# Kernel optimization log

Hardware: AMD Instinct MI355X
Metric: run time of the kernel (lower is better)

## Reference

```python
import jax, jax.numpy as jnp
import numpy as np

B, N, D = 4, 2048, 1024
WIN, K, ALPHA = 4, 8, 0.3


def setup_inputs() -> dict:
    key = jax.random.key(0)
    ks = jax.random.split(key, 16)
    s_d = 1.0 / np.sqrt(D)
    s_2d = 1.0 / np.sqrt(2 * D)
    inp = {
        'mu': jax.random.normal(ks[0], (B, N, D), jnp.float32),
        'pheromone': jax.random.uniform(ks[1], (B, N), jnp.float32),
        'Wq': jax.random.normal(ks[2], (D, D), jnp.float32) * s_d,
        'bq': jnp.zeros((D,), jnp.float32),
        'Wk': jax.random.normal(ks[3], (D, D), jnp.float32) * s_d,
        'bk': jnp.zeros((D,), jnp.float32),
        'Wv': jax.random.normal(ks[4], (D, D), jnp.float32) * s_d,
        'bv': jnp.zeros((D,), jnp.float32),
        'Wm1': jax.random.normal(ks[5], (2 * D, D), jnp.float32) * s_2d,
        'bm1': jnp.zeros((D,), jnp.float32),
        'Wm2': jax.random.normal(ks[6], (D, D), jnp.float32) * s_d,
        'bm2': jnp.zeros((D,), jnp.float32),
        'Wo': jax.random.normal(ks[7], (2 * D, D), jnp.float32) * s_2d,
        'bo': jnp.zeros((D,), jnp.float32),
    }
    return inp


def reference(mu, pheromone, Wq, bq, Wk, bk, Wv, bv, Wm1, bm1, Wm2, bm2, Wo, bo):
    # ---- local windowed gather-MLP ----
    padded = jnp.pad(mu, ((0, 0), (WIN, 0), (0, 0)))  # causal left-pad
    neighbors = jnp.stack([padded[:, WIN - w:WIN - w + N, :] for w in range(1, WIN + 1)], axis=2)
    self_exp = jnp.broadcast_to(mu[:, :, None, :], neighbors.shape)
    cat = jnp.concatenate([self_exp, neighbors], axis=-1)
    h = jax.nn.silu(cat @ Wm1 + bm1) @ Wm2 + bm2
    local_msgs = h.mean(axis=2)  # (B,N,D)

    # ---- causal top-k attention with pheromone bias ----
    q = mu @ Wq + bq
    k = mu @ Wk + bk
    v = mu @ Wv + bv
    scale = 1.0 / jnp.sqrt(jnp.asarray(D, mu.dtype))
    scores = jnp.einsum('bnd,bmd->bnm', q, k) * scale  # (B,N,N)
    scores = scores + ALPHA * pheromone[:, None, :]
    row = jnp.arange(N)
    causal = jnp.where(row[None, :] > row[:, None], -jnp.inf, 0.0).astype(mu.dtype)
    scores = scores + causal[None]
    # top-k sparsification (N > K): softmax over the k kept scores, zeros elsewhere
    vals, idx = jax.lax.top_k(scores, K)  # (B,N,K)
    probs = jax.nn.softmax(vals, axis=-1)
    bi = jnp.arange(B)[:, None, None]
    ni = jnp.arange(N)[None, :, None]
    attn = jnp.zeros_like(scores).at[bi, ni, idx].set(probs)
    global_msgs = jnp.einsum('bnm,bmd->bnd', attn, v)

    return jnp.concatenate([local_msgs, global_msgs], axis=-1) @ Wo + bo
```

## Files before the change

### kernel.cpp

```cpp
#include <hip/hip_runtime.h>
#include <hip/hip_bf16.h>
#include <math.h>

#define B_ 4
#define N_ 2048
#define D_ 1024
#define WIN_ 4
#define KTOP 8
#define ALPHA_ 0.3f
#define SCALE_ (1.0f/32.0f)
#define NCH 16
#define INV2048 0.00048828125f

typedef unsigned short ushortT;
typedef _Float16 halfT;
typedef __attribute__((ext_vector_type(8))) _Float16 half8v;
typedef __attribute__((ext_vector_type(4))) float f32x4;

__device__ inline ushortT h2u(halfT h){ union{halfT h; ushortT u;} x; x.h=h; return x.u; }
__device__ inline halfT  u2h(ushortT u){ union{halfT h; ushortT u;} x; x.u=u; return x.h; }
__device__ inline float  uh2f(ushortT u){ return (float)u2h(u); }

__device__ __forceinline__ void gll16(const ushortT* g, ushortT* l) {
    __builtin_amdgcn_global_load_lds(
        (const __attribute__((address_space(1))) void*)g,
        (__attribute__((address_space(3))) void*)l, 16, 0, 0);
}

__global__ __launch_bounds__(256)
void prep_all(const float* __restrict__ mu, const float* __restrict__ Wm1,
              const float* __restrict__ Wm2, const float* __restrict__ Wv,
              const float* __restrict__ Wo, const float* __restrict__ Wq,
              const float* __restrict__ Wk,
              ushortT* __restrict__ mu_a, ushortT* __restrict__ mu_B,
              ushortT* __restrict__ WtF, ushortT* __restrict__ Wt_m2,
              ushortT* __restrict__ Wt_v, ushortT* __restrict__ Wt_o,
              ushortT* __restrict__ WqT_a, ushortT* __restrict__ WqT_B,
              ushortT* __restrict__ WkT_a, ushortT* __restrict__ WkT_B)
{
    const int bid = blockIdx.x;
    if (bid < 8192) {
        size_t base = ((size_t)bid * 256 + threadIdx.x) * 4;
        float4 v = *reinterpret_cast<const float4*>(&mu[base]);
        float vv[4] = {v.x, v.y, v.z, v.w};
        ushort4 pa, pb;
#pragma unroll
        for (int j = 0; j < 4; ++j) {
            float f = vv[j];
            halfT a = (halfT)f;  float r = f - (float)a;
            halfT b = (halfT)(r * 2048.0f);
            ((ushortT*)&pa)[j] = h2u(a); ((ushortT*)&pb)[j] = h2u(b);
        }
        *reinterpret_cast<ushort4*>(&mu_a[base]) = pa;
        *reinterpret_cast<ushort4*>(&mu_B[base]) = pb;
        return;
    }
    __shared__ float t[32][33];
    int b = bid - 8192;
    const float* W; ushortT* Pa; ushortT* Pb = nullptr;
    int K, lb, split = 0;
    if (b < 1024)      { W = Wm1;                       Pa = WtF;                     K = 1024; lb = b; }
    else if (b < 2048) { W = Wm1 + (size_t)1024 * 1024; Pa = WtF + (size_t)1024*1024; K = 1024; lb = b - 1024; }
    else if (b < 3072) { W = Wm2;  Pa = Wt_m2; K = 1024; lb = b - 2048; }
    else if (b < 4096) { W = Wv;   Pa = Wt_v;  K = 1024; lb = b - 3072; }
    else if (b < 6144) { W = Wo;   Pa = Wt_o;  K = 2048; lb = b - 4096; }
    else if (b < 7168) { W = Wq;   Pa = WqT_a; Pb = WqT_B; K = 1024; lb = b - 6144; split = 1; }
    else               { W = Wk;   Pa = WkT_a; Pb = WkT_B; K = 1024; lb = b - 7168; split = 1; }
    const int Nn = 1024;
    const int k0 = (K == 2048) ? (lb & 63) * 32 : (lb & 31) * 32;
    const int n0 = (K == 2048) ? (lb >> 6) * 32 : (lb >> 5) * 32;
    const int tx = threadIdx.x & 31, ty8 = threadIdx.x >> 5;
#pragma unroll
    for (int p = 0; p < 4; ++p) {
        int kk = p * 8 + ty8;
        t[kk][tx] = W[(size_t)(k0 + kk) * Nn + n0 + tx];
    }
    __syncthreads();
#pragma unroll
    for (int p = 0; p < 4; ++p) {
        int nn = p * 8 + ty8;
        float f = t[tx][nn];
        size_t o = (size_t)(n0 + nn) * K + k0 + tx;
        if (split) {
            halfT a = (halfT)f;  float r = f - (float)a;
            halfT bb = (halfT)(r * 2048.0f);
            Pa[o] = h2u(a); Pb[o] = h2u(bb);
        } else {
            Pa[o] = h2u((halfT)f);
        }
    }
}

__device__ __forceinline__ void gemm_core_h(
    const ushortT* __restrict__ A, int lda, const ushortT* __restrict__ Bt, int ldb,
    const float* __restrict__ bias, void* __restrict__ Cout, int ldc, int K,
    int m0, int n0, int outHalf, ushortT* AsL, ushortT* BsL)
{
    const int tid = threadIdx.x;
    const int w = tid >> 6, lane = tid & 63;
    const int wr = w >> 1, wc = w & 1;

    f32x4 acc[4][4];
#pragma unroll
    for (int mi = 0; mi < 4; ++mi)
#pragma unroll
        for (int ni = 0; ni < 4; ++ni) acc[mi][ni] = (f32x4){0.f, 0.f, 0.f, 0.f};

    for (int k0 = 0; k0 < K; k0 += 64) {
#pragma unroll
        for (int it = 0; it < 4; ++it) {
            int idx = tid + it * 256;
            int row = idx >> 3, c = idx & 7;
            int4 va = *reinterpret_cast<const int4*>(&A[(size_t)(m0 + row) * lda + k0 + c * 8]);
            *reinterpret_cast<int4*>(&AsL[row * 72 + c * 8]) = va;
            int4 vb = *reinterpret_cast<const int4*>(&Bt[(size_t)(n0 + row) * ldb + k0 + c * 8]);
            *reinterpret_cast<int4*>(&BsL[row * 72 + c * 8]) = vb;
        }
        __syncthreads();
#pragma unroll
        for (int kh = 0; kh < 2; ++kh) {
            const int ko = kh * 32 + (lane >> 4) * 8;
            const int rr = lane & 15;
            half8v af[4], bf[4];
#pragma unroll
            for (int mi = 0; mi < 4; ++mi)
                af[mi] = *reinterpret_cast<const half8v*>(&AsL[(wr * 64 + mi * 16 + rr) * 72 + ko]);
#pragma unroll
            for (int ni = 0; ni < 4; ++ni)
                bf[ni] = *reinterpret_cast<const half8v*>(&BsL[(wc * 64 + ni * 16 + rr) * 72 + ko]);
#pragma unroll
            for (int mi = 0; mi < 4; ++mi)
#pragma unroll
                for (int ni = 0; ni < 4; ++ni)
                    acc[mi][ni] = __builtin_amdgcn_mfma_f32_16x16x32_f16(
                        af[mi], bf[ni], acc[mi][ni], 0, 0, 0);
        }
        __syncthreads();
    }

    const int r4 = (lane >> 4) * 4, cl = lane & 15;
#pragma unroll
    for (int mi = 0; mi < 4; ++mi)
#pragma unroll
        for (int ni = 0; ni < 4; ++ni) {
            int row = m0 + wr * 64 + mi * 16 + r4;
            int col = n0 + wc * 64 + ni * 16 + cl;
            float bb = bias ? bias[col] : 0.f;
#pragma unroll
            for (int r = 0; r < 4; ++r) {
                float v = acc[mi][ni][r] + bb;
                if (outHalf)
                    ((ushortT*)Cout)[(size_t)(row + r) * ldc + col] = h2u((halfT)v);
                else
                    ((float*)Cout)[(size_t)(row + r) * ldc + col] = v;
            }
        }
}

template<int OUT_HALF>
__global__ __launch_bounds__(256)
void mfma_gemm_h(const ushortT* __restrict__ A, int lda,
                 const ushortT* __restrict__ Bt, int ldb,
                 const float* __restrict__ bias,
                 void* __restrict__ Cout, int ldc, int K)
{
    __shared__ ushortT AsL[128 * 72];
    __shared__ ushortT BsL[128 * 72];
    gemm_core_h(A, lda, Bt, ldb, bias, Cout, ldc, K,
                blockIdx.y * 128, blockIdx.x * 128, OUT_HALF, AsL, BsL);
}

__global__ __launch_bounds__(256)
void gemm_pf_v(const ushortT* __restrict__ mu_a,
               const ushortT* __restrict__ WtF, const ushortT* __restrict__ Wt_v,
               const float* __restrict__ bv,
               float* __restrict__ PF, ushortT* __restrict__ Vb16)
{
    __shared__ ushortT AsL[128 * 72];
    __shared__ ushortT BsL[128 * 72];
    const int bid = blockIdx.x;
    if (bid < 1024) {
        gemm_core_h(mu_a, D_, WtF, D_, (const float*)nullptr, (void*)PF, 2 * D_, D_,
                    (bid >> 4) * 128, (bid & 15) * 128, 0, AsL, BsL);
    } else {
        const int b2 = bid - 1024;
        gemm_core_h(mu_a, D_, Wt_v, D_, bv, (void*)Vb16, D_, D_,
                    (b2 >> 3) * 128, (b2 & 7) * 128, 1, AsL, BsL);
    }
}

__global__ __launch_bounds__(256)
void silu_mean(const float* __restrict__ P, const float* __restrict__ bm1,
               ushortT* __restrict__ Sb)
{
    size_t idx4 = (size_t)blockIdx.x * blockDim.x + threadIdx.x;
    size_t base = idx4 << 2;
    int row = (int)(base >> 10);
    int col = (int)(base & 1023);
    int n = row & (N_ - 1);
    float4 a = *reinterpret_cast<const float4*>(&P[(size_t)row * 2048 + col]);
    float4 bb = *reinterpret_cast<const float4*>(&bm1[col]);
    a.x += bb.x; a.y += bb.y; a.z += bb.z; a.w += bb.w;
    float sx = 0.f, sy = 0.f, sz = 0.f, sw = 0.f;
#pragma unroll
    for (int w = 1; w <= WIN_; ++w) {
        float xx = a.x, xy = a.y, xz = a.z, xw = a.w;
        if (n >= w) {
            const float4 nb = *reinterpret_cast<const float4*>(
                &P[(size_t)(row - w) * 2048 + 1024 + col]);
            xx += nb.x; xy += nb.y; xz += nb.z; xw += nb.w;
        }
        sx += xx / (1.f + __expf(-xx));
        sy += xy / (1.f + __expf(-xy));
        sz += xz / (1.f + __expf(-xz));
        sw += xw / (1.f + __expf(-xw));
    }
    ushort4 o = {h2u((halfT)(sx * 0.25f)), h2u((halfT)(sy * 0.25f)),
                 h2u((halfT)(sz * 0.25f)), h2u((halfT)(sw * 0.25f))};
    *reinterpret_cast<ushort4*>(&Sb[base]) = o;
}

__device__ inline void topk_insert(float (&tv)[KTOP], int (&ti)[KTOP], float s, int m)
{
    if ((s > tv[KTOP-1]) || (s == tv[KTOP-1] && m < ti[KTOP-1])) {
        float cs = s; int ci = m;
#pragma unroll
        for (int q = 0; q < KTOP; ++q) {
            bool beats = (cs > tv[q]) || (cs == tv[q] && ci < ti[q]);
            if (beats) { float t0 = tv[q]; int t1 = ti[q];
                         tv[q] = cs; ti[q] = ci; cs = t0; ci = t1; }
        }
    }
}

#define SPLIT3H_COMPUTE(Tb, wr, wc, lane, acc0, acc1)                           \
    {                                                                           \
        const int rr_ = (lane) & 15, q_ = (lane) >> 4;                          \
        const int Rb0_ = (wc) * 32 + rr_;                                       \
        const int Rb1_ = Rb0_ + 16;                                             \
        half8v ba0_ = *reinterpret_cast<const half8v*>(                         \
            &Tb[2 * 4096 + Rb0_ * 32 + ((q_ ^ ((Rb0_ >> 1) & 3)) << 3)]);       \
        half8v ba1_ = *reinterpret_cast<const half8v*>(                         \
            &Tb[2 * 4096 + Rb1_ * 32 + ((q_ ^ ((Rb1_ >> 1) & 3)) << 3)]);       \
        half8v bB0_ = *reinterpret_cast<const half8v*>(                         \
            &Tb[3 * 4096 + Rb0_ * 32 + ((q_ ^ ((Rb0_ >> 1) & 3)) << 3)]);       \
        half8v bB1_ = *reinterpret_cast<const half8v*>(                         \
            &Tb[3 * 4096 + Rb1_ * 32 + ((q_ ^ ((Rb1_ >> 1) & 3)) << 3)]);       \
        _Pragma("unroll")                                                       \
        for (int mi_ = 0; mi_ < 4; ++mi_) {                                     \
            const int Ra_ = (wr) * 64 + mi_ * 16 + rr_;                         \
            const int sw_ = (q_ ^ ((Ra_ >> 1) & 3)) << 3;                       \
            half8v aA_ = *reinterpret_cast<const half8v*>(&Tb[Ra_ * 32 + sw_]); \
            acc0[mi_][0] = __builtin_amdgcn_mfma_f32_16x16x32_f16(              \
                aA_, ba0_, acc0[mi_][0], 0, 0, 0);                              \
            acc0[mi_][1] = __builtin_amdgcn_mfma_f32_16x16x32_f16(              \
                aA_, ba1_, acc0[mi_][1], 0, 0, 0);                              \
            acc1[mi_][0] = __builtin_amdgcn_mfma_f32_16x16x32_f16(              \
                aA_, bB0_, acc1[mi_][0], 0, 0, 0);                              \
            acc1[mi_][1] = __builtin_amdgcn_mfma_f32_16x16x32_f16(              \
                aA_, bB1_, acc1[mi_][1], 0, 0, 0);                              \
        }                                                                       \
        _Pragma("unroll")                                                       \
        for (int mi_ = 0; mi_ < 4; ++mi_) {                                     \
            const int Ra_ = (wr) * 64 + mi_ * 16 + rr_;                         \
            const int sw_ = (q_ ^ ((Ra_ >> 1) & 3)) << 3;                       \
            half8v aB_ = *reinterpret_cast<const half8v*>(                      \
                &Tb[4096 + Ra_ * 32 + sw_]);                                    \
            acc1[mi_][0] = __builtin_amdgcn_mfma_f32_16x16x32_f16(              \
                aB_, ba0_, acc1[mi_][0], 0, 0, 0);                              \
            acc1[mi_][1] = __builtin_amdgcn_mfma_f32_16x16x32_f16(              \
                aB_, ba1_, acc1[mi_][1], 0, 0, 0);                              \
        }                                                                       \
    }

#define STAGE4(lb, koff)                                                        \
    {                                                                           \
        gll16(gp + goff + (koff), lb);                                          \
        gll16(gp + goff + (koff) + 16 * D_, (lb) + 512);                        \
        gll16(gp + goff + (koff) + 32 * D_, (lb) + 1024);                       \
        gll16(gp + goff + (koff) + 48 * D_, (lb) + 1536);                       \
    }

__global__ __launch_bounds__(512, 2)
void mid_all(const ushortT* __restrict__ A0, const ushortT* __restrict__ A1,
             const ushortT* __restrict__ QWa, const ushortT* __restrict__ QWB,
             const ushortT* __restrict__ KWa, const ushortT* __restrict__ KWB,
             const float* __restrict__ bq, const float* __restrict__ bk,
             ushortT* __restrict__ Qa, ushortT* __restrict__ QB,
             ushortT* __restrict__ Ka, ushortT* __restrict__ KB,
             const ushortT* __restrict__ Sb, const ushortT* __restrict__ Wt_m2,
             const float* __restrict__ bm2, ushortT* __restrict__ CCb)
{
    __shared__ ushortT SMEM[18432];

    const int tid = threadIdx.x;
    const int wid = tid >> 6, lane = tid & 63;

    if (blockIdx.x >= 1024) {
        const int t = blockIdx.x - 1024;
        const int m0 = (t >> 3) * 128;
        const int n0 = (t & 7) * 128;
        ushortT* AsL = SMEM;
        ushortT* BsL = SMEM + 9216;
        const int wr = wid >> 2, wc = wid & 3;

        f32x4 acc[4][2];
#pragma unroll
        for (int mi = 0; mi < 4; ++mi) { acc[mi][0] = (f32x4){0,0,0,0}; acc[mi][1] = (f32x4){0,0,0,0}; }

        for (int k0 = 0; k0 < D_; k0 += 64) {
#pragma unroll
            for (int it = 0; it < 2; ++it) {
                int idx = tid + it * 512;
                int row = idx >> 3, c = idx & 7;
                int4 va = *reinterpret_cast<const int4*>(&Sb[(size_t)(m0 + row) * D_ + k0 + c * 8]);
                *reinterpret_cast<int4*>(&AsL[row * 72 + c * 8]) = va;
                int4 vb = *reinterpret_cast<const int4*>(&Wt_m2[(size_t)(n0 + row) * D_ + k0 + c * 8]);
                *reinterpret_cast<int4*>(&BsL[row * 72 + c * 8]) = vb;
            }
            __syncthreads();
#pragma unroll
            for (int kh = 0; kh < 2; ++kh) {
                const int ko = kh * 32 + (lane >> 4) * 8;
                const int rr = lane & 15;
                half8v af[4], bf[2];
#pragma unroll
                for (int mi = 0; mi < 4; ++mi)
                    af[mi] = *reinterpret_cast<const half8v*>(&AsL[(wr * 64 + mi * 16 + rr) * 72 + ko]);
#pragma unroll
                for (int ni = 0; ni < 2; ++ni)
                    bf[ni] = *reinterpret_cast<const half8v*>(&BsL[(wc * 32 + ni * 16 + rr) * 72 + ko]);
#pragma unroll
                for (int mi = 0; mi < 4; ++mi)
#pragma unroll
                    for (int ni = 0; ni < 2; ++ni)
                        acc[mi][ni] = __builtin_amdgcn_mfma_f32_16x16x32_f16(
                            af[mi], bf[ni], acc[mi][ni], 0, 0, 0);
            }
            __syncthreads();
        }

        const int r4 = (lane >> 4) * 4, cl = lane & 15;
#pragma unroll
        for (int mi = 0; mi < 4; ++mi)
#pragma unroll
            for (int ni = 0; ni < 2; ++ni) {
                int col = n0 + wc * 32 + ni * 16 + cl;
                float bb = bm2[col];
#pragma unroll
                for (int r = 0; r < 4; ++r) {
                    int row = m0 + wr * 64 + mi * 16 + r4 + r;
                    CCb[(size_t)row * 2048 + col] = h2u((halfT)(acc[mi][ni][r] + bb));
                }
            }
        return;
    }

    ushortT* TT = SMEM;
    const int half = blockIdx.x >> 9;
    int lin = blockIdx.x & 511;
    lin = (lin & 7) * 64 + (lin >> 3);
    const int m0 = (lin >> 3) * 128;
    const int n0 = (lin & 7) * 128;

    const ushortT* B0 = half ? KWa : QWa;
    const ushortT* B1 = half ? KWB : QWB;
    const float* bias = half ? bk : bq;
    ushortT* Pa = half ? Ka : Qa;
    ushortT* Pb = half ? KB : QB;

    const int wr = wid >> 2, wc = wid & 3;
    const int pl = wid >> 1;
    const int hb = (wid & 1) * 64;
    const ushortT* gp = (pl == 0) ? A0 : (pl == 1) ? A1 : (pl == 2) ? B0 : B1;
    const int rbase = (pl < 2 ? m0 : n0) + hb + (lane >> 2);
    const int cg8 = ((lane & 3) ^ ((lane >> 3) & 3)) << 3;
    const size_t goff = (size_t)rbase * D_ + cg8;
    ushortT* lb0 = &TT[pl * 4096 + hb * 32];

    f32x4 acc0[4][2], acc1[4][2];
#pragma unroll
    for (int mi = 0; mi < 4; ++mi) {
        acc0[mi][0] = (f32x4){0,0,0,0}; acc0[mi][1] = (f32x4){0,0,0,0};
        acc1[mi][0] = (f32x4){0,0,0,0}; acc1[mi][1] = (f32x4){0,0,0,0};
    }

    for (int ks = 0; ks < 32; ++ks) {
        STAGE4(lb0, (size_t)ks * 32)
        __syncthreads();
        __builtin_amdgcn_s_setprio(1);
        SPLIT3H_COMPUTE(TT, wr, wc, lane, acc0, acc1)
        __builtin_amdgcn_s_setprio(0);
        __syncthreads();
    }

    const int r4 = (lane >> 4) * 4, cl = lane & 15;
#pragma unroll
    for (int mi = 0; mi < 4; ++mi)
#pragma unroll
        for (int ni = 0; ni < 2; ++ni) {
            int col = n0 + wc * 32 + ni * 16 + cl;
            float bb = bias[col];
#pragma unroll
            for (int r = 0; r < 4; ++r) {
                int row = m0 + wr * 64 + mi * 16 + r4 + r;
                float v = acc0[mi][ni][r] + INV2048 * acc1[mi][ni][r] + bb;
                halfT a = (halfT)v;  float r1 = v - (float)a;
                halfT b = (halfT)(r1 * 2048.0f);
                size_t o = (size_t)row * D_ + col;
                Pa[o] = h2u(a); Pb[o] = h2u(b);
            }
        }
}

__global__ __launch_bounds__(512, 2)
void attn_scores_h(const ushortT* __restrict__ Qa, const ushortT* __restrict__ QB,
                   const ushortT* __restrict__ Ka, const ushortT* __restrict__ KB,
                   const float* __restrict__ pher,
                   float* __restrict__ WV, int* __restrict__ WI)
{
    __shared__ ushortT TT[16384];
    __shared__ float Ps[128];
    __shared__ float PV[32 * 4 * 8];
    __shared__ int   PI[32 * 4 * 8];
    float* MV = reinterpret_cast<float*>(&TT[0]);
    int*   MI = reinterpret_cast<int*>((char*)&TT[0] + 16384);

    int lin = blockIdx.y * 136 + blockIdx.x;
    lin = (lin & 7) * 68 + (lin >> 3);
    const int b = lin / 136;
    const int xy = lin - b * 136;
    int g = 0;
    while ((g + 1) * (g + 2) / 2 <= xy) ++g;
    const int ch = xy - g * (g + 1) / 2;
    const int n0 = g * 128;
    const int m0 = ch * 128;
    const size_t bN = (size_t)b * N_;

    const int tid = threadIdx.x;
    const int wid = tid >> 6, lane = tid & 63;
    const int wr = wid >> 2, wc = wid & 3;

    if (tid < 128) Ps[tid] = pher[bN + m0 + tid];

    const int pl = wid >> 1;
    const int hb = (wid & 1) * 64;
    const ushortT* gp = (pl == 0) ? Qa : (pl == 1) ? QB : (pl == 2) ? Ka : KB;
    const size_t rbase = bN + (pl < 2 ? n0 : m0) + hb + (lane >> 2);
    const int cg8 = ((lane & 3) ^ ((lane >> 3) & 3)) << 3;
    const size_t goff = rbase * (size_t)D_ + cg8;
    ushortT* lb0 = &TT[pl * 4096 + hb * 32];

    f32x4 acc0[4][2], acc1[4][2];
#pragma unroll
    for (int mi = 0; mi < 4; ++mi) {
        acc0[mi][0] = (f32x4){0,0,0,0}; acc0[mi][1] = (f32x4){0,0,0,0};
        acc1[mi][0] = (f32x4){0,0,0,0}; acc1[mi][1] = (f32x4){0,0,0,0};
    }

    for (int ks = 0; ks < 32; ++ks) {
        STAGE4(lb0, (size_t)ks * 32)
        __syncthreads();
        __builtin_amdgcn_s_setprio(1);
        SPLIT3H_COMPUTE(TT, wr, wc, lane, acc0, acc1)
        __builtin_amdgcn_s_setprio(0);
        __syncthreads();
    }

    const int r4 = (lane >> 4) * 4, cl = lane & 15;
    for (int p = 0; p < 4; ++p) {
        __syncthreads();
        if (wr == (p >> 1)) {
#pragma unroll
            for (int mi2 = 0; mi2 < 2; ++mi2) {
                const int mi = (p & 1) * 2 + mi2;
#pragma unroll
                for (int ni = 0; ni < 2; ++ni) {
                    int col = wc * 32 + ni * 16 + cl;
                    int m = m0 + col;
#pragma unroll
                    for (int r = 0; r < 4; ++r) {
                        int rloc = mi2 * 16 + r4 + r;
                        int n = n0 + p * 32 + rloc;
                        bool ok = (m <= n);
                        float sc = acc0[mi][ni][r] + INV2048 * acc1[mi][ni][r];
                        MV[rloc * 128 + col] = ok ? (sc * SCALE_ + ALPHA_ * Ps[col])
                                                  : -INFINITY;
                        MI[rloc * 128 + col] = ok ? m : 0x7fffffff;
                    }
                }
            }
        }
        __syncthreads();
        if (tid < 128) {
            const int row = tid >> 2, q4 = tid & 3;
            float tv[KTOP]; int ti[KTOP];
#pragma unroll
            for (int j = 0; j < KTOP; ++j) { tv[j] = -INFINITY; ti[j] = 0x7fffffff; }
            for (int j = 0; j < 32; ++j) {
                float s2 = MV[row * 128 + q4 * 32 + j];
                if (s2 == -INFINITY) continue;
                topk_insert(tv, ti, s2, MI[row * 128 + q4 * 32 + j]);
            }
#pragma unroll
            for (int j = 0; j < KTOP; ++j) {
                PV[(row * 4 + q4) * 8 + j] = tv[j];
                PI[(row * 4 + q4) * 8 + j] = ti[j];
            }
        }
        __syncthreads();
        if (tid < 32) {
            float tv[KTOP]; int ti[KTOP];
#pragma unroll
            for (int j = 0; j < KTOP; ++j) { tv[j] = -INFINITY; ti[j] = 0x7fffffff; }
            for (int i = 0; i < 32; ++i) {
                float s2 = PV[tid * 32 + i];
                if (s2 == -INFINITY) continue;
                topk_insert(tv, ti, s2, PI[tid * 32 + i]);
            }
            int n = n0 + p * 32 + tid;
            size_t base = ((bN + n) * NCH + ch) * 8;
#pragma unroll
            for (int j = 0; j < KTOP; ++j) { WV[base + j] = tv[j]; WI[base + j] = ti[j]; }
        }
    }
}

__global__ __launch_bounds__(256)
void attn_merge(const float* __restrict__ WV, const int* __restrict__ WI,
                const ushortT* __restrict__ V, ushortT* __restrict__ CCb)
{
    __shared__ float CV[4][128];
    __shared__ int   CI[4][128];
    __shared__ float Pp[4][KTOP];
    __shared__ int   Pi[4][KTOP];

    const int tid  = threadIdx.x;
    const int wv   = tid >> 6;
    const int lane = tid & 63;
    const int rid  = blockIdx.x * 4 + wv;
    const int b    = rid >> 11;
    const int n    = rid & (N_ - 1);
    const int ncand = ((n >> 7) + 1) * 8;
    const size_t cbase = (size_t)rid * (NCH * 8);

#pragma unroll
    for (int t = 0; t < 2; ++t) {
        int i = lane + t * 64;
        if (i < ncand) { CV[wv][i] = WV[cbase + i]; CI[wv][i] = WI[cbase + i]; }
        else           { CV[wv][i] = -INFINITY;     CI[wv][i] = 0x7fffffff;   }
    }
    __syncthreads();

    if (lane == 0) {
        float tv[KTOP]; int ti[KTOP];
#pragma unroll
        for (int j = 0; j < KTOP; ++j) { tv[j] = -INFINITY; ti[j] = 0x7fffffff; }
        for (int i = 0; i < 128; ++i) {
            float s = CV[wv][i];
            if (s == -INFINITY) continue;
            topk_insert(tv, ti, s, CI[wv][i]);
        }
        float mx = tv[0];
        float e[KTOP]; float sum = 0.f;
#pragma unroll
        for (int j = 0; j < KTOP; ++j) {
            e[j] = (tv[j] == -INFINITY) ? 0.f : __expf(tv[j] - mx);
            sum += e[j];
        }
        float inv = 1.f / sum;
#pragma unroll
        for (int j = 0; j < KTOP; ++j) {
            Pp[wv][j] = e[j] * inv;
            Pi[wv][j] = (tv[j] == -INFINITY) ? 0 : ti[j];
        }
    }
    __syncthreads();

    const size_t vbase = (size_t)b * N_ * D_;
#pragma unroll
    for (int it = 0; it < 2; ++it) {
        int c8 = (it * 64 + lane) * 8;
        float o[8];
#pragma unroll
        for (int u = 0; u < 8; ++u) o[u] = 0.f;
#pragma unroll
        for (int j = 0; j < KTOP; ++j) {
            float p = Pp[wv][j];
            ushort4 v0 = *reinterpret_cast<const ushort4*>(
                &V[vbase + (size_t)Pi[wv][j] * D_ + c8]);
            ushort4 v1 = *reinterpret_cast<const ushort4*>(
                &V[vbase + (size_t)Pi[wv][j] * D_ + c8 + 4]);
            o[0] = fmaf(p, uh2f(v0.x), o[0]); o[1] = fmaf(p, uh2f(v0.y), o[1]);
            o[2] = fmaf(p, uh2f(v0.z), o[2]); o[3] = fmaf(p, uh2f(v0.w), o[3]);
            o[4] = fmaf(p, uh2f(v1.x), o[4]); o[5] = fmaf(p, uh2f(v1.y), o[5]);
            o[6] = fmaf(p, uh2f(v1.z), o[6]); o[7] = fmaf(p, uh2f(v1.w), o[7]);
        }
        ushort4 ob0 = {h2u((halfT)o[0]), h2u((halfT)o[1]), h2u((halfT)o[2]), h2u((halfT)o[3])};
        ushort4 ob1 = {h2u((halfT)o[4]), h2u((halfT)o[5]), h2u((halfT)o[6]), h2u((halfT)o[7])};
        *reinterpret_cast<ushort4*>(&CCb[(size_t)rid * 2048 + 1024 + c8]) = ob0;
        *reinterpret_cast<ushort4*>(&CCb[(size_t)rid * 2048 + 1024 + c8 + 4]) = ob1;
    }
}

extern "C" void kernel_launch(void* const* d_in, const int* in_sizes, int n_in,
                              void* d_out, int out_size, void* d_ws, size_t ws_size,
                              hipStream_t stream)
{
    const float* mu   = (const float*)d_in[0];
    const float* pher = (const float*)d_in[1];
    const float* Wq   = (const float*)d_in[2];
    const float* bq   = (const float*)d_in[3];
    const float* Wk   = (const float*)d_in[4];
    const float* bk   = (const float*)d_in[5];
    const float* Wv   = (const float*)d_in[6];
    const float* bv   = (const float*)d_in[7];
    const float* Wm1  = (const float*)d_in[8];
    const float* bm1  = (const float*)d_in[9];
    const float* Wm2  = (const float*)d_in[10];
    const float* bm2  = (const float*)d_in[11];
    const float* Wo   = (const float*)d_in[12];
    const float* bo   = (const float*)d_in[13];
    float* out = (float*)d_out;
    float* ws  = (float*)d_ws;

    const size_t SZ  = (size_t)B_ * N_ * D_;
    const size_t MEG = 1024 * 1024;
    const int M = B_ * N_;

    ushortT* CCb  = (ushortT*)ws;
    float*   PF   = ws + SZ;
    ushortT* Qa   = (ushortT*)(ws + SZ);
    ushortT* QB   = Qa + SZ;
    ushortT* Ka   = (ushortT*)(ws + 2 * SZ);
    ushortT* KB   = Ka + SZ;
    ushortT* mu_a = (ushortT*)(ws + 3 * SZ);
    ushortT* mu_B = mu_a + SZ;
    ushortT* Sb   = (ushortT*)(ws + 4 * SZ);
    float*   WVb  = (float*)(ws + 4 * SZ);
    int*     WIb  = (int*)(WVb + MEG);
    ushortT* Vb16 = (ushortT*)(ws + 4 * SZ + 4 * MEG);
    ushortT* U    = (ushortT*)(ws + 4 * SZ + 8 * MEG);
    ushortT* WtF  = U;
    ushortT* Wt_m2 = U + 2 * MEG;
    ushortT* Wt_v  = U + 3 * MEG;
    ushortT* WqT_a = U + 4 * MEG;        ushortT* WqT_B = U + 5 * MEG;
    ushortT* WkT_a = U + 6 * MEG;        ushortT* WkT_B = U + 7 * MEG;
    ushortT* Wt_o  = U + 8 * MEG;

    dim3 blk256(256), blk512(512);
    dim3 gD(8, 64);

    hipLaunchKernelGGL(prep_all, dim3(16384), blk256, 0, stream,
                       mu, Wm1, Wm2, Wv, Wo, Wq, Wk,
                       mu_a, mu_B, WtF, Wt_m2, Wt_v, Wt_o,
                       WqT_a, WqT_B, WkT_a, WkT_B);
    hipLaunchKernelGGL(gemm_pf_v, dim3(1536), blk256, 0, stream,
                       mu_a, WtF, Wt_v, bv, PF, Vb16);
    hipLaunchKernelGGL(silu_mean, dim3(SZ / 4 / 256), blk256, 0, stream, PF, bm1, Sb);
    hipLaunchKernelGGL(mid_all, dim3(1536), blk512, 0, stream,
                       mu_a, mu_B, WqT_a, WqT_B, WkT_a, WkT_B,
                       bq, bk, Qa, QB, Ka, KB,
                       Sb, Wt_m2, bm2, CCb);
    hipLaunchKernelGGL(attn_scores_h, dim3(136, B_), blk512, 0, stream,
                       Qa, QB, Ka, KB, pher, WVb, WIb);
    hipLaunchKernelGGL(attn_merge, dim3(M / 4), blk256, 0, stream, WVb, WIb, Vb16, CCb);
    hipLaunchKernelGGL((mfma_gemm_h<0>), gD, blk256, 0, stream,
                       CCb, 2 * D_, Wt_o, 2048, bo, (void*)out, D_, 2 * D_);

    (void)in_sizes; (void)n_in; (void)out_size; (void)ws_size;
}
```

Before: 739.1 us.

## Load MFMA operands directly from global memory instead of staging through LDS

```diff
diff --git a/kernel.cpp b/kernel.cpp
--- a/kernel.cpp
+++ b/kernel.cpp
@@ -20,12 +20,6 @@
 __device__ inline ushortT h2u(halfT h){ union{halfT h; ushortT u;} x; x.h=h; return x.u; }
 __device__ inline halfT  u2h(ushortT u){ union{halfT h; ushortT u;} x; x.u=u; return x.h; }
 __device__ inline float  uh2f(ushortT u){ return (float)u2h(u); }
-
-__device__ __forceinline__ void gll16(const ushortT* g, ushortT* l) {
-    __builtin_amdgcn_global_load_lds(
-        (const __attribute__((address_space(1))) void*)g,
-        (__attribute__((address_space(3))) void*)l, 16, 0, 0);
-}
 
 __global__ __launch_bounds__(256)
 void prep_all(const float* __restrict__ mu, const float* __restrict__ Wm1,
@@ -233,52 +227,37 @@
     }
 }
 
-#define SPLIT3H_COMPUTE(Tb, wr, wc, lane, acc0, acc1)                           \
+#define SPLIT3H_DIRECT(PA0, PA1, PB0, PB1, oA, oBv0, oBv1, kk, acc0, acc1)      \
     {                                                                           \
-        const int rr_ = (lane) & 15, q_ = (lane) >> 4;                          \
-        const int Rb0_ = (wc) * 32 + rr_;                                       \
-        const int Rb1_ = Rb0_ + 16;                                             \
-        half8v ba0_ = *reinterpret_cast<const half8v*>(                         \
-            &Tb[2 * 4096 + Rb0_ * 32 + ((q_ ^ ((Rb0_ >> 1) & 3)) << 3)]);       \
-        half8v ba1_ = *reinterpret_cast<const half8v*>(                         \
-            &Tb[2 * 4096 + Rb1_ * 32 + ((q_ ^ ((Rb1_ >> 1) & 3)) << 3)]);       \
-        half8v bB0_ = *reinterpret_cast<const half8v*>(                         \
-            &Tb[3 * 4096 + Rb0_ * 32 + ((q_ ^ ((Rb0_ >> 1) & 3)) << 3)]);       \
-        half8v bB1_ = *reinterpret_cast<const half8v*>(                         \
-            &Tb[3 * 4096 + Rb1_ * 32 + ((q_ ^ ((Rb1_ >> 1) & 3)) << 3)]);       \
+        half8v ba0_ = *reinterpret_cast<const half8v*>(&PB0[oBv0 + (kk)]);      \
+        half8v ba1_ = *reinterpret_cast<const half8v*>(&PB0[oBv1 + (kk)]);      \
+        half8v bB0_ = *reinterpret_cast<const half8v*>(&PB1[oBv0 + (kk)]);      \
+        half8v bB1_ = *reinterpret_cast<const half8v*>(&PB1[oBv1 + (kk)]);      \
+        half8v aA_[4], aB_[4];                                                  \
+        _Pragma("unroll")                                                       \
+        for (int mi_ = 0; mi_ < 4; ++mi_)                                       \
+            aA_[mi_] = *reinterpret_cast<const half8v*>(&PA0[oA[mi_] + (kk)]);  \
+        _Pragma("unroll")                                                       \
+        for (int mi_ = 0; mi_ < 4; ++mi_)                                       \
+            aB_[mi_] = *reinterpret_cast<const half8v*>(&PA1[oA[mi_] + (kk)]);  \
         _Pragma("unroll")                                                       \
         for (int mi_ = 0; mi_ < 4; ++mi_) {                                     \
-            const int Ra_ = (wr) * 64 + mi_ * 16 + rr_;                         \
-            const int sw_ = (q_ ^ ((Ra_ >> 1) & 3)) << 3;                       \
-            half8v aA_ = *reinterpret_cast<const half8v*>(&Tb[Ra_ * 32 + sw_]); \
             acc0[mi_][0] = __builtin_amdgcn_mfma_f32_16x16x32_f16(              \
-                aA_, ba0_, acc0[mi_][0], 0, 0, 0);                              \
+                aA_[mi_], ba0_, acc0[mi_][0], 0, 0, 0);                         \
             acc0[mi_][1] = __builtin_amdgcn_mfma_f32_16x16x32_f16(              \
-                aA_, ba1_, acc0[mi_][1], 0, 0, 0);                              \
+                aA_[mi_], ba1_, acc0[mi_][1], 0, 0, 0);                         \
             acc1[mi_][0] = __builtin_amdgcn_mfma_f32_16x16x32_f16(              \
-                aA_, bB0_, acc1[mi_][0], 0, 0, 0);                              \
+                aA_[mi_], bB0_, acc1[mi_][0], 0, 0, 0);                         \
             acc1[mi_][1] = __builtin_amdgcn_mfma_f32_16x16x32_f16(              \
-                aA_, bB1_, acc1[mi_][1], 0, 0, 0);                              \
+                aA_[mi_], bB1_, acc1[mi_][1], 0, 0, 0);                         \
         }                                                                       \
         _Pragma("unroll")                                                       \
         for (int mi_ = 0; mi_ < 4; ++mi_) {                                     \
-            const int Ra_ = (wr) * 64 + mi_ * 16 + rr_;                         \
-            const int sw_ = (q_ ^ ((Ra_ >> 1) & 3)) << 3;                       \
-            half8v aB_ = *reinterpret_cast<const half8v*>(                      \
-                &Tb[4096 + Ra_ * 32 + sw_]);                                    \
             acc1[mi_][0] = __builtin_amdgcn_mfma_f32_16x16x32_f16(              \
-                aB_, ba0_, acc1[mi_][0], 0, 0, 0);                              \
+                aB_[mi_], ba0_, acc1[mi_][0], 0, 0, 0);                         \
             acc1[mi_][1] = __builtin_amdgcn_mfma_f32_16x16x32_f16(              \
-                aB_, ba1_, acc1[mi_][1], 0, 0, 0);                              \
+                aB_[mi_], ba1_, acc1[mi_][1], 0, 0, 0);                         \
         }                                                                       \
-    }
-
-#define STAGE4(lb, koff)                                                        \
-    {                                                                           \
-        gll16(gp + goff + (koff), lb);                                          \
-        gll16(gp + goff + (koff) + 16 * D_, (lb) + 512);                        \
-        gll16(gp + goff + (koff) + 32 * D_, (lb) + 1024);                       \
-        gll16(gp + goff + (koff) + 48 * D_, (lb) + 1536);                       \
     }
 
 __global__ __launch_bounds__(512, 2)
@@ -356,7 +335,6 @@
         return;
     }
 
-    ushortT* TT = SMEM;
     const int half = blockIdx.x >> 9;
     int lin = blockIdx.x & 511;
     lin = (lin & 7) * 64 + (lin >> 3);
@@ -370,13 +348,13 @@
     ushortT* Pb = half ? KB : QB;
 
     const int wr = wid >> 2, wc = wid & 3;
-    const int pl = wid >> 1;
-    const int hb = (wid & 1) * 64;
-    const ushortT* gp = (pl == 0) ? A0 : (pl == 1) ? A1 : (pl == 2) ? B0 : B1;
-    const int rbase = (pl < 2 ? m0 : n0) + hb + (lane >> 2);
-    const int cg8 = ((lane & 3) ^ ((lane >> 3) & 3)) << 3;
-    const size_t goff = (size_t)rbase * D_ + cg8;
-    ushortT* lb0 = &TT[pl * 4096 + hb * 32];
+    const int rr = lane & 15, q8 = (lane >> 4) * 8;
+    size_t oA[4];
+#pragma unroll
+    for (int mi = 0; mi < 4; ++mi)
+        oA[mi] = (size_t)(m0 + wr * 64 + mi * 16 + rr) * D_ + q8;
+    const size_t oBv0 = (size_t)(n0 + wc * 32 + rr) * D_ + q8;
+    const size_t oBv1 = oBv0 + (size_t)16 * D_;
 
     f32x4 acc0[4][2], acc1[4][2];
 #pragma unroll
@@ -386,12 +364,8 @@
     }
 
     for (int ks = 0; ks < 32; ++ks) {
-        STAGE4(lb0, (size_t)ks * 32)
-        __syncthreads();
-        __builtin_amdgcn_s_setprio(1);
-        SPLIT3H_COMPUTE(TT, wr, wc, lane, acc0, acc1)
-        __builtin_amdgcn_s_setprio(0);
-        __syncthreads();
+        const int kk = ks * 32;
+        SPLIT3H_DIRECT(A0, A1, B0, B1, oA, oBv0, oBv1, kk, acc0, acc1)
     }
 
     const int r4 = (lane >> 4) * 4, cl = lane & 15;
@@ -419,12 +393,11 @@
                    const float* __restrict__ pher,
                    float* __restrict__ WV, int* __restrict__ WI)
 {
-    __shared__ ushortT TT[16384];
+    __shared__ float MV[32 * 128];
+    __shared__ int   MI[32 * 128];
     __shared__ float Ps[128];
     __shared__ float PV[32 * 4 * 8];
     __shared__ int   PI[32 * 4 * 8];
-    float* MV = reinterpret_cast<float*>(&TT[0]);
-    int*   MI = reinterpret_cast<int*>((char*)&TT[0] + 16384);
 
     int lin = blockIdx.y * 136 + blockIdx.x;
     lin = (lin & 7) * 68 + (lin >> 3);
@@ -443,13 +416,13 @@
 
     if (tid < 128) Ps[tid] = pher[bN + m0 + tid];
 
-    const int pl = wid >> 1;
-    const int hb = (wid & 1) * 64;
-    const ushortT* gp = (pl == 0) ? Qa : (pl == 1) ? QB : (pl == 2) ? Ka : KB;
-    const size_t rbase = bN + (pl < 2 ? n0 : m0) + hb + (lane >> 2);
-    const int cg8 = ((lane & 3) ^ ((lane >> 3) & 3)) << 3;
-    const size_t goff = rbase * (size_t)D_ + cg8;
-    ushortT* lb0 = &TT[pl * 4096 + hb * 32];
+    const int rr = lane & 15, q8 = (lane >> 4) * 8;
+    size_t oA[4];
+#pragma unroll
+    for (int mi = 0; mi < 4; ++mi)
+        oA[mi] = (bN + n0 + wr * 64 + mi * 16 + rr) * (size_t)D_ + q8;
+    const size_t oBv0 = (bN + m0 + wc * 32 + rr) * (size_t)D_ + q8;
+    const size_t oBv1 = oBv0 + (size_t)16 * D_;
 
     f32x4 acc0[4][2], acc1[4][2];
 #pragma unroll
@@ -459,12 +432,8 @@
     }
 
     for (int ks = 0; ks < 32; ++ks) {
-        STAGE4(lb0, (size_t)ks * 32)
-        __syncthreads();
-        __builtin_amdgcn_s_setprio(1);
-        SPLIT3H_COMPUTE(TT, wr, wc, lane, acc0, acc1)
-        __builtin_amdgcn_s_setprio(0);
-        __syncthreads();
+        const int kk = ks * 32;
+        SPLIT3H_DIRECT(Qa, QB, Ka, KB, oA, oBv0, oBv1, kk, acc0, acc1)
     }
 
     const int r4 = (lane >> 4) * 4, cl = lane & 15;
```

Result: slower. 1.304 ms (+76.4%).
